# Kernel tuning notes

Hardware: AMD Instinct MI355X
Metric: run time of the kernel (lower is better)

The kernel has to match this reference:

```python
import jax, jax.numpy as jnp
import numpy as np

B, C, H, W = 8, 128, 48, 48
GROUPS = 32
EPS = 1e-5


def group_norm(x, w, b):
    # x: [B,C,H,W] -> normalize within 32 groups over (C//G, H, W)
    xg = x.reshape(B, GROUPS, C // GROUPS, H, W)
    mu = xg.mean(axis=(2, 3, 4), keepdims=True)
    var = xg.var(axis=(2, 3, 4), keepdims=True)
    xg = (xg - mu) * jax.lax.rsqrt(var + EPS)
    return xg.reshape(B, C, H, W) * w[None, :, None, None] + b[None, :, None, None]


def conv1x1(x, w, b):
    # pointwise conv: [B,C,H,W], w: [Cout,Cin], b: [Cout]
    return jnp.einsum('oc,bchw->bohw', w, x) + b[None, :, None, None]


def setup_inputs() -> dict:
    key = jax.random.key(0)
    ks = jax.random.split(key, 6)
    s = 1.0 / np.sqrt(C)
    return {
        'x': jax.random.normal(ks[0], (B, C, H, W), jnp.float32),
        'gn_w': jnp.ones((C,), jnp.float32),
        'gn_b': jnp.zeros((C,), jnp.float32),
        'wq': jax.random.normal(ks[1], (C, C), jnp.float32) * s,
        'bq': jnp.zeros((C,), jnp.float32),
        'wk': jax.random.normal(ks[2], (C, C), jnp.float32) * s,
        'bk': jnp.zeros((C,), jnp.float32),
        'wv': jax.random.normal(ks[3], (C, C), jnp.float32) * s,
        'bv': jnp.zeros((C,), jnp.float32),
        'wo': jax.random.normal(ks[4], (C, C), jnp.float32) * s,
        'bo': jnp.zeros((C,), jnp.float32),
    }


def reference(x, gn_w, gn_b, wq, bq, wk, bk, wv, bv, wo, bo):
    xn = group_norm(x, gn_w, gn_b)
    q = conv1x1(xn, wq, bq)
    k = conv1x1(xn, wk, bk)
    v = conv1x1(xn, wv, bv)
    # scores: [B,H,W,I,J]
    scores = jnp.einsum('bchw,bcij->bhwij', q, k) / jnp.sqrt(jnp.float32(C))
    # NOTE: original calls F.softmax with no dim; torch picks dim=1 (the query-H axis)
    attn = jax.nn.softmax(scores, axis=1)
    ctx = jnp.einsum('bhwnm,bcnm->bchw', attn, v)
    return x + conv1x1(ctx, wo, bo)
```

## Files before the change

### kernel.cpp

```cpp
#include <hip/hip_runtime.h>
#include <hip/hip_bf16.h>

typedef short s16x8 __attribute__((ext_vector_type(8)));
typedef float f32x4 __attribute__((ext_vector_type(4)));
typedef int   i32x4 __attribute__((ext_vector_type(4)));
typedef unsigned short u16;

#define BB 8
#define CC 128
#define HH 48
#define WW 48
#define NN 2304
#define SCALE_L2E 0.12751744f
#define SZ_MAP (BB*CC*NN)
#define NSPLIT 2
#define TILES_PER (18/NSPLIT)

__device__ inline u16 f2bf(float f) {
    unsigned u = __builtin_bit_cast(unsigned, f);
    u = (u + 0x7FFFu + ((u >> 16) & 1u)) >> 16;
    return (u16)u;
}
__device__ inline float bf2f(u16 h) {
    unsigned u = ((unsigned)h) << 16;
    return __builtin_bit_cast(float, u);
}

#define MFMA(a, b, c) __builtin_amdgcn_mfma_f32_16x16x32_bf16(a, b, c, 0, 0, 0)
#define DPP_ROR_ADD(x, N) { \
    int yi_ = __builtin_amdgcn_update_dpp(0, __builtin_bit_cast(int, x), 0x120 | (N), 0xf, 0xf, true); \
    x += __builtin_bit_cast(float, yi_); }

__global__ __launch_bounds__(256) void gnprep_kernel(
        const float* __restrict__ x, const float* __restrict__ gw,
        const float* __restrict__ gb, u16* __restrict__ xnT,
        const float* __restrict__ wq, const float* __restrict__ wk,
        const float* __restrict__ wv_, const float* __restrict__ wo,
        u16* __restrict__ w16) {
    int tid = threadIdx.x;
    if (blockIdx.x >= 256) {
        int i = (blockIdx.x - 256) * 256 + tid;
        int m = i >> 14, r = i & 16383;
        const float* src = (m == 0) ? wq : (m == 1) ? wk : (m == 2) ? wv_ : wo;
        w16[i] = f2bf(src[r]);
        return;
    }
    int b = blockIdx.x & 7, g = blockIdx.x >> 3;
    const float* xb = x + ((size_t)b * CC + g * 4) * NN;
    float v[4][9];
    float s = 0.f, ss = 0.f;
#pragma unroll
    for (int c = 0; c < 4; ++c)
#pragma unroll
        for (int k = 0; k < 9; ++k) {
            float t = xb[c * NN + tid + k * 256];
            v[c][k] = t; s += t; ss += t * t;
        }
#pragma unroll
    for (int o = 32; o > 0; o >>= 1) { s += __shfl_down(s, o); ss += __shfl_down(ss, o); }
    __shared__ float red[8];
    __shared__ float stats[2];
    int wid = tid >> 6;
    if ((tid & 63) == 0) { red[wid * 2] = s; red[wid * 2 + 1] = ss; }
    __syncthreads();
    if (tid == 0) {
        float S = 0.f, SS = 0.f;
        for (int i = 0; i < 4; ++i) { S += red[i * 2]; SS += red[i * 2 + 1]; }
        float mu = S * (1.f / 9216.f);
        float var = SS * (1.f / 9216.f) - mu * mu;
        stats[0] = mu;
        stats[1] = rsqrtf(var + 1e-5f);
    }
    __syncthreads();
    float mu = stats[0], rs = stats[1];
    float sc[4], bi[4];
#pragma unroll
    for (int c = 0; c < 4; ++c) {
        sc[c] = gw[g * 4 + c] * rs;
        bi[c] = gb[g * 4 + c] - mu * sc[c];
    }
#pragma unroll
    for (int k = 0; k < 9; ++k) {
        int n = tid + k * 256;
        ushort4 o;
        o.x = f2bf(v[0][k] * sc[0] + bi[0]);
        o.y = f2bf(v[1][k] * sc[1] + bi[1]);
        o.z = f2bf(v[2][k] * sc[2] + bi[2]);
        o.w = f2bf(v[3][k] * sc[3] + bi[3]);
        *(ushort4*)(xnT + ((size_t)b * NN + n) * CC + g * 4) = o;
    }
}

__global__ __launch_bounds__(256) void qkv_kernel(
        const u16* __restrict__ xnT, const u16* __restrict__ w16,
        const float* __restrict__ bq, const float* __restrict__ bk,
        const float* __restrict__ bv,
        u16* __restrict__ qT, u16* __restrict__ kt2, u16* __restrict__ vt2) {
    int b = blockIdx.x, n0 = blockIdx.y * 128, z = blockIdx.z;
    int tid = threadIdx.x, lane = tid & 63, wvw = tid >> 6;
    int l15 = lane & 15, l4 = lane >> 4;
    const u16* xb = xnT + (size_t)b * NN * CC;

    if (z == 0) {
        const u16* w16q = w16;
        const u16* w16k = w16 + 16384;
        u16* kb = kt2 + (size_t)b * NN * CC;
        s16x8 xa[2][4];
#pragma unroll
        for (int mf = 0; mf < 2; ++mf)
#pragma unroll
            for (int ks = 0; ks < 4; ++ks)
                xa[mf][ks] = *(const s16x8*)(xb + (size_t)(n0 + wvw * 32 + mf * 16 + l15) * CC + ks * 32 + l4 * 8);
        int chunk = blockIdx.y * 4 + wvw;
#pragma unroll 2
        for (int nf = 0; nf < 8; ++nf) {
            f32x4 aq[2] = {}, ak[2] = {};
#pragma unroll
            for (int ks = 0; ks < 4; ++ks) {
                s16x8 fq = *(const s16x8*)(w16q + (nf * 16 + l15) * CC + ks * 32 + l4 * 8);
                s16x8 fk = *(const s16x8*)(w16k + (nf * 16 + l15) * CC + ks * 32 + l4 * 8);
#pragma unroll
                for (int mf = 0; mf < 2; ++mf) {
                    aq[mf] = MFMA(fq, xa[mf][ks], aq[mf]);
                    ak[mf] = MFMA(fk, xa[mf][ks], ak[mf]);
                }
            }
            int cob = nf * 16 + l4 * 4;
            float4 bq4 = *(const float4*)(bq + cob);
            float4 bk4 = *(const float4*)(bk + cob);
#pragma unroll
            for (int mf = 0; mf < 2; ++mf) {
                int n = n0 + wvw * 32 + mf * 16 + l15;
                ushort4 qo;
                qo.x = f2bf((aq[mf][0] + bq4.x) * SCALE_L2E);
                qo.y = f2bf((aq[mf][1] + bq4.y) * SCALE_L2E);
                qo.z = f2bf((aq[mf][2] + bq4.z) * SCALE_L2E);
                qo.w = f2bf((aq[mf][3] + bq4.w) * SCALE_L2E);
                *(ushort4*)(qT + ((size_t)b * NN + n) * CC + cob) = qo;
                int n5 = mf * 16 + l15;
                int slot = ((n5 & 4) << 2) + ((n5 & 24) >> 1) + (n5 & 3);
                ushort4 ko;
                ko.x = f2bf(ak[mf][0] + bk4.x);
                ko.y = f2bf(ak[mf][1] + bk4.y);
                ko.z = f2bf(ak[mf][2] + bk4.z);
                ko.w = f2bf(ak[mf][3] + bk4.w);
                *(ushort4*)(kb + (size_t)chunk * 4096 + (cob >> 5) * 1024 + slot * 32 + (cob & 31)) = ko;
            }
        }
    } else {
        const u16* w16v = w16 + 2 * 16384;
        u16* vb = vt2 + (size_t)b * NN * CC;
        s16x8 wa[2][4];
#pragma unroll
        for (int mf = 0; mf < 2; ++mf)
#pragma unroll
            for (int ks = 0; ks < 4; ++ks)
                wa[mf][ks] = *(const s16x8*)(w16v + (wvw * 32 + mf * 16 + l15) * CC + ks * 32 + l4 * 8);
        float bvl[2];
        bvl[0] = bv[wvw * 32 + l15];
        bvl[1] = bv[wvw * 32 + 16 + l15];
#pragma unroll 2
        for (int nf = 0; nf < 8; ++nf) {
            f32x4 av[2] = {};
#pragma unroll
            for (int ks = 0; ks < 4; ++ks) {
                s16x8 xf = *(const s16x8*)(xb + (size_t)(n0 + nf * 16 + l15) * CC + ks * 32 + l4 * 8);
#pragma unroll
                for (int mf = 0; mf < 2; ++mf) av[mf] = MFMA(xf, wa[mf][ks], av[mf]);
            }
            int chunk = blockIdx.y * 4 + (nf >> 1);
            int nlo = (nf & 1) * 16 + l4 * 4;
#pragma unroll
            for (int mf = 0; mf < 2; ++mf) {
                ushort4 vo;
                vo.x = f2bf(av[mf][0] + bvl[mf]);
                vo.y = f2bf(av[mf][1] + bvl[mf]);
                vo.z = f2bf(av[mf][2] + bvl[mf]);
                vo.w = f2bf(av[mf][3] + bvl[mf]);
                *(ushort4*)(vb + (size_t)chunk * 4096 + (wvw * 2 + mf) * 512 + l15 * 32 + nlo) = vo;
            }
        }
    }
}

__global__ __launch_bounds__(256, 3) void attn_kernel(
        const u16* __restrict__ qT, const u16* __restrict__ kt2,
        const u16* __restrict__ vt2, u16* __restrict__ part) {
    int b = blockIdx.x, w = blockIdx.y, sp = blockIdx.z;
    int tid = threadIdx.x, lane = tid & 63, wvw = tid >> 6;
    int l15 = lane & 15, l4 = lane >> 4;
    __shared__ float red[4 * 48 * 36];
    __shared__ u16 qlds[48 * 128];

    const u16* qb = qT + (size_t)b * NN * CC;
    const u16* kb = kt2 + (size_t)b * NN * CC;
    const u16* vb = vt2 + (size_t)b * NN * CC;

#pragma unroll
    for (int pp = 0; pp < 3; ++pp) {
        int pid = pp * 4 + wvw;
        int hf = pid >> 2, ks = pid & 3;
        s16x8 q = *(const s16x8*)(qb + (size_t)((hf * 16 + l15) * WW + w) * CC + ks * 32 + l4 * 8);
        int m = (ks * 4 + l4) ^ (l15 & 7);
        *(s16x8*)(qlds + (hf * 16 + l15) * 128 + m * 8) = q;
    }
    __syncthreads();

    f32x4 cacc[8][3] = {};

    const int tbase = sp * TILES_PER;
#pragma unroll 1
    for (int t = tbase; t < tbase + TILES_PER; ++t) {
        asm volatile("" ::: "memory");
        const u16* cb = kb + (size_t)(t * 4 + wvw) * 4096;
        const u16* cv = vb + (size_t)(t * 4 + wvw) * 4096;
        f32x4 sf[2][3] = {};
        __builtin_amdgcn_s_setprio(1);
#pragma unroll
        for (int ks = 0; ks < 4; ++ks) {
            s16x8 kf0 = *(const s16x8*)(cb + ks * 1024 + l15 * 32 + l4 * 8);
            s16x8 kf1 = *(const s16x8*)(cb + ks * 1024 + (16 + l15) * 32 + l4 * 8);
#pragma unroll
            for (int hf = 0; hf < 3; ++hf) {
                s16x8 q = *(const s16x8*)(qlds + (hf * 16 + l15) * 128
                                          + (((ks * 4 + l4) ^ (l15 & 7)) * 8));
                sf[0][hf] = MFMA(kf0, q, sf[0][hf]);
                sf[1][hf] = MFMA(kf1, q, sf[1][hf]);
            }
        }
        __builtin_amdgcn_s_setprio(0);
        float pe[2][3][4];
#pragma unroll
        for (int mf = 0; mf < 2; ++mf)
#pragma unroll
            for (int hf = 0; hf < 3; ++hf)
#pragma unroll
                for (int r = 0; r < 4; ++r) pe[mf][hf][r] = __builtin_amdgcn_exp2f(sf[mf][hf][r]);
        float den[2][4];
#pragma unroll
        for (int mf = 0; mf < 2; ++mf)
#pragma unroll
            for (int r = 0; r < 4; ++r)
                den[mf][r] = pe[mf][0][r] + pe[mf][1][r] + pe[mf][2][r];
#pragma unroll
        for (int mf = 0; mf < 2; ++mf)
#pragma unroll
            for (int r = 0; r < 4; ++r) {
                DPP_ROR_ADD(den[mf][r], 1);
                DPP_ROR_ADD(den[mf][r], 2);
                DPP_ROR_ADD(den[mf][r], 4);
                DPP_ROR_ADD(den[mf][r], 8);
            }
        float rd[2][4];
#pragma unroll
        for (int mf = 0; mf < 2; ++mf)
#pragma unroll
            for (int r = 0; r < 4; ++r) rd[mf][r] = __builtin_amdgcn_rcpf(den[mf][r]);
        s16x8 pbf[3];
#pragma unroll
        for (int hf = 0; hf < 3; ++hf) {
            unsigned u0, u1, u2, u3;
            float a0 = pe[0][hf][0] * rd[0][0], a1 = pe[0][hf][1] * rd[0][1];
            float a2 = pe[0][hf][2] * rd[0][2], a3 = pe[0][hf][3] * rd[0][3];
            float a4 = pe[1][hf][0] * rd[1][0], a5 = pe[1][hf][1] * rd[1][1];
            float a6 = pe[1][hf][2] * rd[1][2], a7 = pe[1][hf][3] * rd[1][3];
            asm("v_cvt_pk_bf16_f32 %0, %1, %2" : "=v"(u0) : "v"(a0), "v"(a1));
            asm("v_cvt_pk_bf16_f32 %0, %1, %2" : "=v"(u1) : "v"(a2), "v"(a3));
            asm("v_cvt_pk_bf16_f32 %0, %1, %2" : "=v"(u2) : "v"(a4), "v"(a5));
            asm("v_cvt_pk_bf16_f32 %0, %1, %2" : "=v"(u3) : "v"(a6), "v"(a7));
            i32x4 bb2 = { (int)u0, (int)u1, (int)u2, (int)u3 };
            pbf[hf] = __builtin_bit_cast(s16x8, bb2);
        }
        __builtin_amdgcn_s_setprio(1);
#pragma unroll
        for (int cf = 0; cf < 8; ++cf) {
            s16x8 vf = *(const s16x8*)(cv + cf * 512 + l15 * 32 + l4 * 8);
#pragma unroll
            for (int hf = 0; hf < 3; ++hf)
                cacc[cf][hf] = MFMA(vf, pbf[hf], cacc[cf][hf]);
        }
        __builtin_amdgcn_s_setprio(0);
    }

#pragma unroll
    for (int s = 0; s < 4; ++s) {
        if (s) __syncthreads();
#pragma unroll
        for (int q = 0; q < 4; ++q) {
            if (((q - wvw) & 3) == s) {
#pragma unroll
                for (int i = 0; i < 2; ++i) {
                    int cf = 2 * q + i;
#pragma unroll
                    for (int hf = 0; hf < 3; ++hf) {
                        int addr = q * 1728 + (hf * 16 + l15) * 36 + i * 16 + 4 * l4;
                        f32x4* pp = (f32x4*)&red[addr];
                        if (s == 0) *pp = cacc[cf][hf];
                        else { f32x4 tv = *pp; tv += cacc[cf][hf]; *pp = tv; }
                    }
                }
            }
        }
    }
    __syncthreads();
    u16* po = part + (size_t)(b * NSPLIT + sp) * NN * CC;
#pragma unroll
    for (int pass = 0; pass < 12; ++pass) {
        int h = pass * 4 + l4;
        int c = wvw * 32 + l15 * 2;
        float2 v2 = *(float2*)&red[wvw * 1728 + h * 36 + l15 * 2];
        unsigned pk;
        asm("v_cvt_pk_bf16_f32 %0, %1, %2" : "=v"(pk) : "v"(v2.x), "v"(v2.y));
        *(unsigned*)(po + (size_t)(h * WW + w) * CC + c) = pk;
    }
}

__global__ __launch_bounds__(256) void out_kernel(
        const u16* __restrict__ part, const u16* __restrict__ w16o,
        const float* __restrict__ bo, const float* __restrict__ x,
        float* __restrict__ out) {
    int b = blockIdx.x, n0 = blockIdx.y * 128;
    int tid = threadIdx.x, lane = tid & 63, wvw = tid >> 6;
    int l15 = lane & 15, l4 = lane >> 4;
    const u16* pb = part + (size_t)b * NSPLIT * NN * CC;
    s16x8 bfr[2][4];
#pragma unroll
    for (int nf = 0; nf < 2; ++nf)
#pragma unroll
        for (int ks = 0; ks < 4; ++ks) {
            size_t off = (size_t)(n0 + wvw * 32 + nf * 16 + l15) * CC + ks * 32 + l4 * 8;
            s16x8 v0 = *(const s16x8*)(pb + off);
            s16x8 v1 = *(const s16x8*)(pb + (size_t)NN * CC + off);
            s16x8 o;
#pragma unroll
            for (int j = 0; j < 8; ++j)
                o[j] = (short)f2bf(bf2f((u16)v0[j]) + bf2f((u16)v1[j]));
            bfr[nf][ks] = o;
        }
#pragma unroll 2
    for (int mf = 0; mf < 8; ++mf) {
        s16x8 af[4];
#pragma unroll
        for (int ks = 0; ks < 4; ++ks)
            af[ks] = *(const s16x8*)(w16o + (mf * 16 + l15) * CC + ks * 32 + l4 * 8);
        f32x4 acc[2] = {};
#pragma unroll
        for (int ks = 0; ks < 4; ++ks)
#pragma unroll
            for (int nf = 0; nf < 2; ++nf)
                acc[nf] = MFMA(af[ks], bfr[nf][ks], acc[nf]);
#pragma unroll
        for (int nf = 0; nf < 2; ++nf)
#pragma unroll
            for (int r = 0; r < 4; ++r) {
                int co = mf * 16 + l4 * 4 + r;
                int n = n0 + wvw * 32 + nf * 16 + l15;
                size_t idx = ((size_t)b * CC + co) * NN + n;
                out[idx] = acc[nf][r] + bo[co] + x[idx];
            }
    }
}

extern "C" void kernel_launch(void* const* d_in, const int* in_sizes, int n_in,
                              void* d_out, int out_size, void* d_ws, size_t ws_size,
                              hipStream_t stream) {
    const float* x  = (const float*)d_in[0];
    const float* gw = (const float*)d_in[1];
    const float* gb = (const float*)d_in[2];
    const float* wq = (const float*)d_in[3];
    const float* bq = (const float*)d_in[4];
    const float* wk = (const float*)d_in[5];
    const float* bk = (const float*)d_in[6];
    const float* wv_ = (const float*)d_in[7];
    const float* bv = (const float*)d_in[8];
    const float* wo = (const float*)d_in[9];
    const float* bo = (const float*)d_in[10];

    u16* ws   = (u16*)d_ws;
    u16* xnT  = ws;
    u16* qT   = ws + (size_t)SZ_MAP;
    u16* kt2  = ws + (size_t)2 * SZ_MAP;
    u16* vt2  = ws + (size_t)3 * SZ_MAP;
    u16* part = ws + (size_t)4 * SZ_MAP;
    u16* w16  = ws + (size_t)(4 + NSPLIT) * SZ_MAP;
    float* out = (float*)d_out;

    gnprep_kernel<<<512, 256, 0, stream>>>(x, gw, gb, xnT, wq, wk, wv_, wo, w16);
    qkv_kernel<<<dim3(8, 18, 2), 256, 0, stream>>>(xnT, w16, bq, bk, bv, qT, kt2, vt2);
    attn_kernel<<<dim3(8, WW, NSPLIT), 256, 0, stream>>>(qT, kt2, vt2, part);
    out_kernel<<<dim3(8, 18), 256, 0, stream>>>(part, w16 + 3 * 16384, bo, x, out);
}
```

Measured before the change: 77.06 us.

## Split QKV and output projection across more blocks, vectorize output stores

The Q and K projections now run in separate z-blocks, and the output projection is split into two channel halves. This raises the block count on the GPU for better occupancy. The out kernel swaps its MFMA operands so each lane holds four consecutive spatial positions, which allows float4 loads of x and float4 stores of out. In the attention loop, the full memory clobber is replaced by a register-only asm barrier so loads can be scheduled more freely. The cost is that the out kernel repeats the partial-sum reduction in both halves, and the xn fragments are loaded twice.

After: 70.48 us (median of 2 runs). 8.5% less time.

```diff
diff --git a/kernel.cpp b/kernel.cpp
--- a/kernel.cpp
+++ b/kernel.cpp
@@ -103,31 +103,24 @@
 
     if (z == 0) {
         const u16* w16q = w16;
-        const u16* w16k = w16 + 16384;
-        u16* kb = kt2 + (size_t)b * NN * CC;
         s16x8 xa[2][4];
 #pragma unroll
         for (int mf = 0; mf < 2; ++mf)
 #pragma unroll
             for (int ks = 0; ks < 4; ++ks)
                 xa[mf][ks] = *(const s16x8*)(xb + (size_t)(n0 + wvw * 32 + mf * 16 + l15) * CC + ks * 32 + l4 * 8);
-        int chunk = blockIdx.y * 4 + wvw;
 #pragma unroll 2
         for (int nf = 0; nf < 8; ++nf) {
-            f32x4 aq[2] = {}, ak[2] = {};
+            f32x4 aq[2] = {};
 #pragma unroll
             for (int ks = 0; ks < 4; ++ks) {
                 s16x8 fq = *(const s16x8*)(w16q + (nf * 16 + l15) * CC + ks * 32 + l4 * 8);
-                s16x8 fk = *(const s16x8*)(w16k + (nf * 16 + l15) * CC + ks * 32 + l4 * 8);
-#pragma unroll
-                for (int mf = 0; mf < 2; ++mf) {
+#pragma unroll
+                for (int mf = 0; mf < 2; ++mf)
                     aq[mf] = MFMA(fq, xa[mf][ks], aq[mf]);
-                    ak[mf] = MFMA(fk, xa[mf][ks], ak[mf]);
-                }
             }
             int cob = nf * 16 + l4 * 4;
             float4 bq4 = *(const float4*)(bq + cob);
-            float4 bk4 = *(const float4*)(bk + cob);
 #pragma unroll
             for (int mf = 0; mf < 2; ++mf) {
                 int n = n0 + wvw * 32 + mf * 16 + l15;
@@ -137,6 +130,32 @@
                 qo.z = f2bf((aq[mf][2] + bq4.z) * SCALE_L2E);
                 qo.w = f2bf((aq[mf][3] + bq4.w) * SCALE_L2E);
                 *(ushort4*)(qT + ((size_t)b * NN + n) * CC + cob) = qo;
+            }
+        }
+    } else if (z == 1) {
+        const u16* w16k = w16 + 16384;
+        u16* kb = kt2 + (size_t)b * NN * CC;
+        s16x8 xa[2][4];
+#pragma unroll
+        for (int mf = 0; mf < 2; ++mf)
+#pragma unroll
+            for (int ks = 0; ks < 4; ++ks)
+                xa[mf][ks] = *(const s16x8*)(xb + (size_t)(n0 + wvw * 32 + mf * 16 + l15) * CC + ks * 32 + l4 * 8);
+        int chunk = blockIdx.y * 4 + wvw;
+#pragma unroll 2
+        for (int nf = 0; nf < 8; ++nf) {
+            f32x4 ak[2] = {};
+#pragma unroll
+            for (int ks = 0; ks < 4; ++ks) {
+                s16x8 fk = *(const s16x8*)(w16k + (nf * 16 + l15) * CC + ks * 32 + l4 * 8);
+#pragma unroll
+                for (int mf = 0; mf < 2; ++mf)
+                    ak[mf] = MFMA(fk, xa[mf][ks], ak[mf]);
+            }
+            int cob = nf * 16 + l4 * 4;
+            float4 bk4 = *(const float4*)(bk + cob);
+#pragma unroll
+            for (int mf = 0; mf < 2; ++mf) {
                 int n5 = mf * 16 + l15;
                 int slot = ((n5 & 4) << 2) + ((n5 & 24) >> 1) + (n5 & 3);
                 ushort4 ko;
@@ -209,9 +228,10 @@
     f32x4 cacc[8][3] = {};
 
     const int tbase = sp * TILES_PER;
+    int qoff = 0;
 #pragma unroll 1
     for (int t = tbase; t < tbase + TILES_PER; ++t) {
-        asm volatile("" ::: "memory");
+        asm volatile("" : "+v"(qoff));
         const u16* cb = kb + (size_t)(t * 4 + wvw) * 4096;
         const u16* cv = vb + (size_t)(t * 4 + wvw) * 4096;
         f32x4 sf[2][3] = {};
@@ -222,7 +242,7 @@
             s16x8 kf1 = *(const s16x8*)(cb + ks * 1024 + (16 + l15) * 32 + l4 * 8);
 #pragma unroll
             for (int hf = 0; hf < 3; ++hf) {
-                s16x8 q = *(const s16x8*)(qlds + (hf * 16 + l15) * 128
+                s16x8 q = *(const s16x8*)(qlds + qoff + (hf * 16 + l15) * 128
                                           + (((ks * 4 + l4) ^ (l15 & 7)) * 8));
                 sf[0][hf] = MFMA(kf0, q, sf[0][hf]);
                 sf[1][hf] = MFMA(kf1, q, sf[1][hf]);
@@ -319,7 +339,7 @@
         const u16* __restrict__ part, const u16* __restrict__ w16o,
         const float* __restrict__ bo, const float* __restrict__ x,
         float* __restrict__ out) {
-    int b = blockIdx.x, n0 = blockIdx.y * 128;
+    int b = blockIdx.x, n0 = blockIdx.y * 128, zh = blockIdx.z;
     int tid = threadIdx.x, lane = tid & 63, wvw = tid >> 6;
     int l15 = lane & 15, l4 = lane >> 4;
     const u16* pb = part + (size_t)b * NSPLIT * NN * CC;
@@ -337,8 +357,9 @@
                 o[j] = (short)f2bf(bf2f((u16)v0[j]) + bf2f((u16)v1[j]));
             bfr[nf][ks] = o;
         }
-#pragma unroll 2
-    for (int mf = 0; mf < 8; ++mf) {
+#pragma unroll
+    for (int mi = 0; mi < 4; ++mi) {
+        int mf = zh * 4 + mi;
         s16x8 af[4];
 #pragma unroll
         for (int ks = 0; ks < 4; ++ks)
@@ -348,16 +369,21 @@
         for (int ks = 0; ks < 4; ++ks)
 #pragma unroll
             for (int nf = 0; nf < 2; ++nf)
-                acc[nf] = MFMA(af[ks], bfr[nf][ks], acc[nf]);
-#pragma unroll
-        for (int nf = 0; nf < 2; ++nf)
-#pragma unroll
-            for (int r = 0; r < 4; ++r) {
-                int co = mf * 16 + l4 * 4 + r;
-                int n = n0 + wvw * 32 + nf * 16 + l15;
-                size_t idx = ((size_t)b * CC + co) * NN + n;
-                out[idx] = acc[nf][r] + bo[co] + x[idx];
-            }
+                acc[nf] = MFMA(bfr[nf][ks], af[ks], acc[nf]);
+        int co = mf * 16 + l15;
+        float bol = bo[co];
+#pragma unroll
+        for (int nf = 0; nf < 2; ++nf) {
+            int n = n0 + wvw * 32 + nf * 16 + l4 * 4;
+            size_t idx = ((size_t)b * CC + co) * NN + n;
+            float4 xr = *(const float4*)(x + idx);
+            float4 o4;
+            o4.x = acc[nf][0] + bol + xr.x;
+            o4.y = acc[nf][1] + bol + xr.y;
+            o4.z = acc[nf][2] + bol + xr.z;
+            o4.w = acc[nf][3] + bol + xr.w;
+            *(float4*)(out + idx) = o4;
+        }
     }
 }
 
@@ -386,7 +412,7 @@
     float* out = (float*)d_out;
 
     gnprep_kernel<<<512, 256, 0, stream>>>(x, gw, gb, xnT, wq, wk, wv_, wo, w16);
-    qkv_kernel<<<dim3(8, 18, 2), 256, 0, stream>>>(xnT, w16, bq, bk, bv, qT, kt2, vt2);
+    qkv_kernel<<<dim3(8, 18, 3), 256, 0, stream>>>(xnT, w16, bq, bk, bv, qT, kt2, vt2);
     attn_kernel<<<dim3(8, WW, NSPLIT), 256, 0, stream>>>(qT, kt2, vt2, part);
-    out_kernel<<<dim3(8, 18), 256, 0, stream>>>(part, w16 + 3 * 16384, bo, x, out);
-}
+    out_kernel<<<dim3(8, 18, 2), 256, 0, stream>>>(part, w16 + 3 * 16384, bo, x, out);
+}
```
